# Optimization experiments

Hardware: AMD Instinct MI355X
Metric: run time of the kernel (lower is better)

The kernel has to match this reference:

```python
import jax, jax.numpy as jnp
import numpy as np

NEG = -1e9  # masked-out (non-edge) additive bias


def _attn_head(seq, bias_mat, W1, a1, b1, a2, b2, W2, bW):
    # seq: [B,N,F]; W1: [F,H]; a1,a2: [H]; W2: [H,K]
    fts = jnp.einsum('bnf,fh->bnh', seq, W1)            # Conv1D(out_sz,1,no bias)
    f1 = jnp.einsum('bnh,h->bn', fts, a1) + b1          # Conv1D(1,1)
    f2 = jnp.einsum('bnh,h->bn', fts, a2) + b2          # Conv1D(1,1)
    logits = f1[:, :, None] + f2[:, None, :]            # [B,N,N] additive attention
    coefs = jax.nn.softmax(jax.nn.leaky_relu(logits, 0.2) + bias_mat, axis=-1)
    vals = jnp.einsum('bnm,bmh->bnh', coefs, fts)       # weighted aggregation
    return jnp.einsum('bnh,hk->bnk', vals, W2) + bW     # bias_add_layer1 (Dense)


def setup_inputs() -> dict:
    B, N, F, H, NH, C = 1, 4096, 512, 64, 8, 40
    key = jax.random.key(0)
    ks = jax.random.split(key, 12)
    seq = jax.random.normal(ks[0], (B, N, F), dtype=jnp.float32)
    adj = jax.random.bernoulli(ks[1], 0.01, (B, N, N)) | jnp.eye(N, dtype=bool)[None]
    bias_mat = jnp.where(adj, 0.0, NEG).astype(jnp.float32)
    s = 0.05
    # 8 stacked first-layer heads (out_sz=H)
    W1 = jax.random.normal(ks[2], (NH, F, H), dtype=jnp.float32) * s
    a1 = jax.random.normal(ks[3], (NH, H), dtype=jnp.float32) * s
    b1 = jnp.zeros((NH,), jnp.float32)
    a2 = jax.random.normal(ks[4], (NH, H), dtype=jnp.float32) * s
    b2 = jnp.zeros((NH,), jnp.float32)
    W2 = jax.random.normal(ks[5], (NH, H, H), dtype=jnp.float32) * s
    bW = jnp.zeros((NH, H), jnp.float32)
    # single output head (out_sz=nb_classes, identity activation)
    Wo1 = jax.random.normal(ks[6], (NH * H, C), dtype=jnp.float32) * s
    ao1 = jax.random.normal(ks[7], (C,), dtype=jnp.float32) * s
    bo1 = jnp.zeros((), jnp.float32)
    ao2 = jax.random.normal(ks[8], (C,), dtype=jnp.float32) * s
    bo2 = jnp.zeros((), jnp.float32)
    Wo2 = jax.random.normal(ks[9], (C, C), dtype=jnp.float32) * s
    bo = jnp.zeros((C,), jnp.float32)
    return dict(seq=seq, bias_mat=bias_mat, W1=W1, a1=a1, b1=b1, a2=a2, b2=b2,
                W2=W2, bW=bW, Wo1=Wo1, ao1=ao1, bo1=bo1, ao2=ao2, bo2=bo2,
                Wo2=Wo2, bo=bo)


def reference(seq, bias_mat, W1, a1, b1, a2, b2, W2, bW,
              Wo1, ao1, bo1, ao2, bo2, Wo2, bo):
    # first layer: 8 heads with elu activation, vmapped over head params
    heads = jax.vmap(
        lambda w1, v1, c1, v2, c2, w2, bw: jax.nn.elu(
            _attn_head(seq, bias_mat, w1, v1, c1, v2, c2, w2, bw))
    )(W1, a1, b1, a2, b2, W2, bW)                        # [NH,B,N,H]
    NH, B, N, H = heads.shape
    h1 = jnp.moveaxis(heads, 0, 2).reshape(B, N, NH * H)  # concat along features
    # output layer: 1 head, identity activation, averaged over n_heads[-1]=1
    out = _attn_head(h1, bias_mat, Wo1, ao1, bo1, ao2, bo2, Wo2, bo)
    return out / 1.0
```

## Files before the change

kernel.cpp:

```cpp
#include <hip/hip_runtime.h>
#include <cstdint>
#include <cstddef>

#define NN 4096
#define FDIM 512
#define HDIM 64
#define NHEAD 8
#define CDIM 40
#define MAXD 256

typedef __attribute__((ext_vector_type(8))) short bf16x8;
typedef __attribute__((ext_vector_type(16))) float f32x16;

__device__ __forceinline__ float wave_max64(float v) {
  for (int o = 32; o; o >>= 1) v = fmaxf(v, __shfl_xor(v, o));
  return v;
}
__device__ __forceinline__ float wave_sum64(float v) {
  for (int o = 32; o; o >>= 1) v += __shfl_xor(v, o);
  return v;
}
__device__ __forceinline__ float readlane_f(float v, int sl) {
  return __uint_as_float((unsigned)__builtin_amdgcn_readlane((int)__float_as_uint(v), sl));
}
__device__ __forceinline__ int readlane_i(int v, int sl) {
  return __builtin_amdgcn_readlane(v, sl);
}
__device__ __forceinline__ unsigned short f2bf(float x) {
  unsigned u = __float_as_uint(x);
  return (unsigned short)((u + 0x7fffu + ((u >> 16) & 1u)) >> 16);
}
__device__ __forceinline__ float bf2f(unsigned short b) {
  return __uint_as_float(((unsigned)b) << 16);
}

__global__ __launch_bounds__(256) void k_prep(
    const float* __restrict__ bias, int* __restrict__ nbr, int* __restrict__ cnt,
    const float* __restrict__ seq, short* __restrict__ Ahi, short* __restrict__ Alo,
    const float* __restrict__ W1, short* __restrict__ Bhi, short* __restrict__ Blo,
    const float* __restrict__ W2, short* __restrict__ W2thi, short* __restrict__ W2tlo,
    const float* __restrict__ Wo1, short* __restrict__ Wo1thi, short* __restrict__ Wo1tlo) {
  __shared__ int wtot[4];
  __shared__ float T[64][65];
  int bx = blockIdx.x, tid = threadIdx.x;
  if (bx < NN) {
    int row = bx;
    int lane = tid & 63, wv = tid >> 6;
    const float4* r = (const float4*)(bias + (size_t)row * NN);
    unsigned mask = 0;
#pragma unroll
    for (int i = 0; i < 4; ++i) {
      float4 v = r[tid * 4 + i];
      mask |= (unsigned)((v.x == 0.f ? 1 : 0) | (v.y == 0.f ? 2 : 0) |
                         (v.z == 0.f ? 4 : 0) | (v.w == 0.f ? 8 : 0)) << (i * 4);
    }
    int c = __popc(mask);
    int pre = c;
#pragma unroll
    for (int o = 1; o < 64; o <<= 1) {
      int u = __shfl_up(pre, o);
      if (lane >= o) pre += u;
    }
    if (lane == 63) wtot[wv] = pre;
    __syncthreads();
    int woff = 0;
#pragma unroll
    for (int w = 0; w < 4; ++w)
      if (w < wv) woff += wtot[w];
    int excl = woff + pre - c;
    int* out = nbr + (size_t)row * MAXD;
    int col0 = tid * 16, k = 0;
#pragma unroll
    for (int i = 0; i < 16; ++i) {
      if ((mask >> i) & 1) {
        int p = excl + k;
        if (p < MAXD) out[p] = col0 + i;
        ++k;
      }
    }
    if (tid == 0) {
      int total = wtot[0] + wtot[1] + wtot[2] + wtot[3];
      cnt[row] = total < MAXD ? total : MAXD;
    }
    return;
  }
  bx -= NN;
  if (bx < 1024) {
    size_t off = (size_t)bx * 2048 + (size_t)tid * 8;
    float4 v0 = *(const float4*)(seq + off);
    float4 v1 = *(const float4*)(seq + off + 4);
    unsigned short h0 = f2bf(v0.x), h1 = f2bf(v0.y), h2 = f2bf(v0.z), h3 = f2bf(v0.w);
    unsigned short h4 = f2bf(v1.x), h5 = f2bf(v1.y), h6 = f2bf(v1.z), h7 = f2bf(v1.w);
    *(uint4*)(Ahi + off) = make_uint4(
        (unsigned)h0 | ((unsigned)h1 << 16), (unsigned)h2 | ((unsigned)h3 << 16),
        (unsigned)h4 | ((unsigned)h5 << 16), (unsigned)h6 | ((unsigned)h7 << 16));
    unsigned short l0 = f2bf(v0.x - bf2f(h0)), l1 = f2bf(v0.y - bf2f(h1));
    unsigned short l2 = f2bf(v0.z - bf2f(h2)), l3 = f2bf(v0.w - bf2f(h3));
    unsigned short l4 = f2bf(v1.x - bf2f(h4)), l5 = f2bf(v1.y - bf2f(h5));
    unsigned short l6 = f2bf(v1.z - bf2f(h6)), l7 = f2bf(v1.w - bf2f(h7));
    *(uint4*)(Alo + off) = make_uint4(
        (unsigned)l0 | ((unsigned)l1 << 16), (unsigned)l2 | ((unsigned)l3 << 16),
        (unsigned)l4 | ((unsigned)l5 << 16), (unsigned)l6 | ((unsigned)l7 << 16));
    return;
  }
  bx -= 1024;
  if (bx < 64) {
    int h = bx >> 3, kb = bx & 7;
    const float* src = W1 + ((size_t)h * FDIM + kb * 64) * HDIM;
#pragma unroll
    for (int q = 0; q < 4; ++q) {
      int fi = q * 256 + tid, kk = fi >> 4, n4 = fi & 15;
      float4 v = *(const float4*)(src + (size_t)kk * HDIM + n4 * 4);
      T[n4 * 4 + 0][kk] = v.x; T[n4 * 4 + 1][kk] = v.y;
      T[n4 * 4 + 2][kk] = v.z; T[n4 * 4 + 3][kk] = v.w;
    }
    __syncthreads();
#pragma unroll
    for (int q = 0; q < 4; ++q) {
      int fi = q * 256 + tid, n = fi >> 4, k4 = fi & 15;
      float a = T[n][k4 * 4], b = T[n][k4 * 4 + 1];
      float c = T[n][k4 * 4 + 2], d = T[n][k4 * 4 + 3];
      size_t o = ((size_t)h * 64 + n) * FDIM + kb * 64 + k4 * 4;
      unsigned short ha = f2bf(a), hb = f2bf(b), hc = f2bf(c), hd = f2bf(d);
      *(short4*)(Bhi + o) = make_short4((short)ha, (short)hb, (short)hc, (short)hd);
      *(short4*)(Blo + o) = make_short4((short)f2bf(a - bf2f(ha)), (short)f2bf(b - bf2f(hb)),
                                        (short)f2bf(c - bf2f(hc)), (short)f2bf(d - bf2f(hd)));
    }
    return;
  }
  bx -= 64;
  if (bx < 8) {
    int h = bx;
    const float* src = W2 + (size_t)h * HDIM * HDIM;
#pragma unroll
    for (int q = 0; q < 4; ++q) {
      int fi = q * 256 + tid, kk = fi >> 4, n4 = fi & 15;
      float4 v = *(const float4*)(src + (size_t)kk * HDIM + n4 * 4);
      T[n4 * 4 + 0][kk] = v.x; T[n4 * 4 + 1][kk] = v.y;
      T[n4 * 4 + 2][kk] = v.z; T[n4 * 4 + 3][kk] = v.w;
    }
    __syncthreads();
#pragma unroll
    for (int q = 0; q < 4; ++q) {
      int fi = q * 256 + tid, n = fi >> 4, k4 = fi & 15;
      float a = T[n][k4 * 4], b = T[n][k4 * 4 + 1];
      float c = T[n][k4 * 4 + 2], d = T[n][k4 * 4 + 3];
      size_t o = (size_t)h * 4096 + (size_t)n * 64 + k4 * 4;
      unsigned short ha = f2bf(a), hb = f2bf(b), hc = f2bf(c), hd = f2bf(d);
      *(short4*)(W2thi + o) = make_short4((short)ha, (short)hb, (short)hc, (short)hd);
      *(short4*)(W2tlo + o) = make_short4((short)f2bf(a - bf2f(ha)), (short)f2bf(b - bf2f(hb)),
                                          (short)f2bf(c - bf2f(hc)), (short)f2bf(d - bf2f(hd)));
    }
    return;
  }
  bx -= 8;
  {
#pragma unroll
    for (int q = 0; q < 16; ++q) {
      int idx = q * 256 + tid;
      int n = bx * 8 + (idx >> 9), k = idx & 511;
      float v = (n < CDIM) ? Wo1[(size_t)k * CDIM + n] : 0.f;
      unsigned short hv = f2bf(v);
      Wo1thi[(size_t)n * FDIM + k] = (short)hv;
      Wo1tlo[(size_t)n * FDIM + k] = (short)f2bf(v - bf2f(hv));
    }
  }
}

__global__ __launch_bounds__(256) void k_gemm(
    const short* __restrict__ Ahi, const short* __restrict__ Alo,
    const short* __restrict__ Bhi, const short* __restrict__ Blo,
    const float* __restrict__ a1, const float* __restrict__ b1,
    const float* __restrict__ a2, const float* __restrict__ b2,
    float* __restrict__ FTS, float* __restrict__ F1t, float* __restrict__ F2t) {
  __shared__ short AH[4][64][16], AL[4][64][16];
  __shared__ short BH[4][128][16], BL[4][128][16];
  const int mtile = blockIdx.x, npair = blockIdx.y;
  const int tid = threadIdx.x, lane = tid & 63, w = tid >> 6;
  const int wm = w >> 1, wn = w & 1;
  const int ml = lane & 31, g = lane >> 5, g8 = g * 8;

  f32x16 acc0, acc1;
#pragma unroll
  for (int r = 0; r < 16; ++r) { acc0[r] = 0.f; acc1[r] = 0.f; }

  const short* Abh = Ahi + (((size_t)mtile * 64) << 9);
  const short* Abl = Alo + (((size_t)mtile * 64) << 9);
  const short* Bbh = Bhi + (((size_t)npair * 128) << 9);
  const short* Bbl = Blo + (((size_t)npair * 128) << 9);

  const int tn = tid >> 3, k8 = tid & 7;
  const int ks = k8 >> 1, ko = (k8 & 1) * 8;
  const size_t so = ((size_t)tn << 9) + (size_t)k8 * 8;

  int4 rah0, rah1, ral0, ral1, rbh0, rbh1, rbh2, rbh3, rbl0, rbl1, rbl2, rbl3;
  {
    rah0 = *(const int4*)(Abh + so);              ral0 = *(const int4*)(Abl + so);
    rah1 = *(const int4*)(Abh + so + (32 << 9));  ral1 = *(const int4*)(Abl + so + (32 << 9));
    rbh0 = *(const int4*)(Bbh + so);              rbl0 = *(const int4*)(Bbl + so);
    rbh1 = *(const int4*)(Bbh + so + (32 << 9));  rbl1 = *(const int4*)(Bbl + so + (32 << 9));
    rbh2 = *(const int4*)(Bbh + so + (64 << 9));  rbl2 = *(const int4*)(Bbl + so + (64 << 9));
    rbh3 = *(const int4*)(Bbh + so + (96 << 9));  rbl3 = *(const int4*)(Bbl + so + (96 << 9));
  }

  const int NCH = FDIM / 64;
  for (int c = 0; c < NCH; ++c) {
    *(int4*)&AH[ks][tn][ko] = rah0;       *(int4*)&AL[ks][tn][ko] = ral0;
    *(int4*)&AH[ks][32 + tn][ko] = rah1;  *(int4*)&AL[ks][32 + tn][ko] = ral1;
    *(int4*)&BH[ks][tn][ko] = rbh0;       *(int4*)&BL[ks][tn][ko] = rbl0;
    *(int4*)&BH[ks][32 + tn][ko] = rbh1;  *(int4*)&BL[ks][32 + tn][ko] = rbl1;
    *(int4*)&BH[ks][64 + tn][ko] = rbh2;  *(int4*)&BL[ks][64 + tn][ko] = rbl2;
    *(int4*)&BH[ks][96 + tn][ko] = rbh3;  *(int4*)&BL[ks][96 + tn][ko] = rbl3;
    __syncthreads();
    if (c + 1 < NCH) {
      size_t o = so + (size_t)(c + 1) * 64;
      rah0 = *(const int4*)(Abh + o);              ral0 = *(const int4*)(Abl + o);
      rah1 = *(const int4*)(Abh + o + (32 << 9));  ral1 = *(const int4*)(Abl + o + (32 << 9));
      rbh0 = *(const int4*)(Bbh + o);              rbl0 = *(const int4*)(Bbl + o);
      rbh1 = *(const int4*)(Bbh + o + (32 << 9));  rbl1 = *(const int4*)(Bbl + o + (32 << 9));
      rbh2 = *(const int4*)(Bbh + o + (64 << 9));  rbl2 = *(const int4*)(Bbl + o + (64 << 9));
      rbh3 = *(const int4*)(Bbh + o + (96 << 9));  rbl3 = *(const int4*)(Bbl + o + (96 << 9));
    }
#pragma unroll
    for (int t = 0; t < 4; ++t) {
      bf16x8 ah = *(const bf16x8*)&AH[t][wm * 32 + ml][g8];
      bf16x8 al = *(const bf16x8*)&AL[t][wm * 32 + ml][g8];
      bf16x8 bh0 = *(const bf16x8*)&BH[t][wn * 64 + ml][g8];
      bf16x8 bl0 = *(const bf16x8*)&BL[t][wn * 64 + ml][g8];
      acc0 = __builtin_amdgcn_mfma_f32_32x32x16_bf16(ah, bh0, acc0, 0, 0, 0);
      acc0 = __builtin_amdgcn_mfma_f32_32x32x16_bf16(al, bh0, acc0, 0, 0, 0);
      acc0 = __builtin_amdgcn_mfma_f32_32x32x16_bf16(ah, bl0, acc0, 0, 0, 0);
      bf16x8 bh1 = *(const bf16x8*)&BH[t][wn * 64 + 32 + ml][g8];
      bf16x8 bl1 = *(const bf16x8*)&BL[t][wn * 64 + 32 + ml][g8];
      acc1 = __builtin_amdgcn_mfma_f32_32x32x16_bf16(ah, bh1, acc1, 0, 0, 0);
      acc1 = __builtin_amdgcn_mfma_f32_32x32x16_bf16(al, bh1, acc1, 0, 0, 0);
      acc1 = __builtin_amdgcn_mfma_f32_32x32x16_bf16(ah, bl1, acc1, 0, 0, 0);
    }
    __syncthreads();
  }

  const int h = npair * 2 + wn;
  const float a1lo = a1[h * 64 + ml], a1hi = a1[h * 64 + 32 + ml];
  const float a2lo = a2[h * 64 + ml], a2hi = a2[h * 64 + 32 + ml];
  const float b1h = b1[h], b2h = b2[h];
  const int row0 = mtile * 64 + wm * 32 + 4 * g;
  const int col0 = npair * 128 + wn * 64 + ml;
#pragma unroll
  for (int r = 0; r < 16; ++r) {
    int row = row0 + (r & 3) + 8 * (r >> 2);
    FTS[(size_t)row * FDIM + col0] = acc0[r];
    FTS[(size_t)row * FDIM + col0 + 32] = acc1[r];
    float p1 = acc0[r] * a1lo + acc1[r] * a1hi;
    float p2 = acc0[r] * a2lo + acc1[r] * a2hi;
#pragma unroll
    for (int o = 1; o < 32; o <<= 1) {
      p1 += __shfl_xor(p1, o);
      p2 += __shfl_xor(p2, o);
    }
    if (ml == 0) {
      F1t[(size_t)row * 8 + h] = p1 + b1h;
      F2t[(size_t)row * 8 + h] = p2 + b2h;
    }
  }
}

__global__ __launch_bounds__(256) void k_agg1(
    const float* __restrict__ FTS, const float* __restrict__ F1t,
    const float* __restrict__ F2t, const int* __restrict__ nbr,
    const int* __restrict__ cnt, short* __restrict__ VALShi,
    short* __restrict__ VALSlo) {
  int wv = threadIdx.x >> 6, lane = threadIdx.x & 63;
  int gw = blockIdx.x * 4 + wv;
  int i = gw >> 1, hg = gw & 1;
  int deg = cnt[i];
  const int* nb = nbr + (size_t)i * MAXD;
  float4 f1v = *(const float4*)(F1t + (size_t)i * 8 + hg * 4);

  float4 p4[4];
  int jreg[4];
  float mx = -1e30f, my = -1e30f, mz = -1e30f, mw = -1e30f;
#pragma unroll
  for (int r = 0; r < 4; ++r) {
    int t = r * 64 + lane;
    jreg[r] = 0;
    p4[r] = make_float4(-1e30f, -1e30f, -1e30f, -1e30f);
    if (t < deg) {
      int j = nb[t];
      jreg[r] = j;
      float4 f2v = *(const float4*)(F2t + (size_t)j * 8 + hg * 4);
      float4 x;
      x.x = f1v.x + f2v.x; x.x = x.x >= 0.f ? x.x : 0.2f * x.x;
      x.y = f1v.y + f2v.y; x.y = x.y >= 0.f ? x.y : 0.2f * x.y;
      x.z = f1v.z + f2v.z; x.z = x.z >= 0.f ? x.z : 0.2f * x.z;
      x.w = f1v.w + f2v.w; x.w = x.w >= 0.f ? x.w : 0.2f * x.w;
      p4[r] = x;
      mx = fmaxf(mx, x.x); my = fmaxf(my, x.y);
      mz = fmaxf(mz, x.z); mw = fmaxf(mw, x.w);
    }
  }
  mx = wave_max64(mx); my = wave_max64(my);
  mz = wave_max64(mz); mw = wave_max64(mw);
  float sx = 0.f, sy = 0.f, sz = 0.f, sw = 0.f;
#pragma unroll
  for (int r = 0; r < 4; ++r) {
    int t = r * 64 + lane;
    float4 e = make_float4(0.f, 0.f, 0.f, 0.f);
    if (t < deg) {
      e.x = __expf(p4[r].x - mx); e.y = __expf(p4[r].y - my);
      e.z = __expf(p4[r].z - mz); e.w = __expf(p4[r].w - mw);
    }
    p4[r] = e;
    sx += e.x; sy += e.y; sz += e.z; sw += e.w;
  }
  sx = wave_sum64(sx); sy = wave_sum64(sy);
  sz = wave_sum64(sz); sw = wave_sum64(sw);

  int q = lane >> 4;
  float invh = (q < 2) ? (q == 0 ? 1.f / sx : 1.f / sy)
                       : (q == 2 ? 1.f / sz : 1.f / sw);

  float4 accA = make_float4(0.f, 0.f, 0.f, 0.f);
  float4 accB = make_float4(0.f, 0.f, 0.f, 0.f);
  const float* Fb = FTS + hg * 256;
#pragma unroll
  for (int r = 0; r < 4; ++r) {
    int base = r * 64;
    if (base >= deg) break;
    int lim = deg - base;
    lim = lim < 64 ? lim : 64;
    int sl = 0;
    for (; sl + 2 <= lim; sl += 2) {
      int j0 = readlane_i(jreg[r], sl);
      int j1 = readlane_i(jreg[r], sl + 1);
      float w00 = readlane_f(p4[r].x, sl),     w01 = readlane_f(p4[r].y, sl);
      float w02 = readlane_f(p4[r].z, sl),     w03 = readlane_f(p4[r].w, sl);
      float w10 = readlane_f(p4[r].x, sl + 1), w11 = readlane_f(p4[r].y, sl + 1);
      float w12 = readlane_f(p4[r].z, sl + 1), w13 = readlane_f(p4[r].w, sl + 1);
      float wA = (q < 2) ? (q == 0 ? w00 : w01) : (q == 2 ? w02 : w03);
      float wB = (q < 2) ? (q == 0 ? w10 : w11) : (q == 2 ? w12 : w13);
      float4 f0 = *(const float4*)(Fb + (size_t)j0 * FDIM + lane * 4);
      float4 f1 = *(const float4*)(Fb + (size_t)j1 * FDIM + lane * 4);
      accA.x += wA * f0.x; accA.y += wA * f0.y; accA.z += wA * f0.z; accA.w += wA * f0.w;
      accB.x += wB * f1.x; accB.y += wB * f1.y; accB.z += wB * f1.z; accB.w += wB * f1.w;
    }
    if (sl < lim) {
      int j0 = readlane_i(jreg[r], sl);
      float w00 = readlane_f(p4[r].x, sl), w01 = readlane_f(p4[r].y, sl);
      float w02 = readlane_f(p4[r].z, sl), w03 = readlane_f(p4[r].w, sl);
      float wA = (q < 2) ? (q == 0 ? w00 : w01) : (q == 2 ? w02 : w03);
      float4 f0 = *(const float4*)(Fb + (size_t)j0 * FDIM + lane * 4);
      accA.x += wA * f0.x; accA.y += wA * f0.y; accA.z += wA * f0.z; accA.w += wA * f0.w;
    }
  }
  float vx = (accA.x + accB.x) * invh, vy = (accA.y + accB.y) * invh;
  float vz = (accA.z + accB.z) * invh, vw = (accA.w + accB.w) * invh;
  unsigned short hx = f2bf(vx), hy = f2bf(vy), hz = f2bf(vz), hw = f2bf(vw);
  size_t o = (size_t)i * FDIM + hg * 256 + lane * 4;
  *(short4*)(VALShi + o) = make_short4((short)hx, (short)hy, (short)hz, (short)hw);
  *(short4*)(VALSlo + o) = make_short4(
      (short)f2bf(vx - bf2f(hx)), (short)f2bf(vy - bf2f(hy)),
      (short)f2bf(vz - bf2f(hz)), (short)f2bf(vw - bf2f(hw)));
}

__global__ __launch_bounds__(256) void k_w2(
    const short* __restrict__ VALShi, const short* __restrict__ VALSlo,
    const short* __restrict__ W2thi, const short* __restrict__ W2tlo,
    const float* __restrict__ bW, short* __restrict__ H1hi, short* __restrict__ H1lo) {
  __shared__ short AH[4][64][16], AL[4][64][16];
  __shared__ short BH[4][64][16], BL[4][64][16];
  const int rb = blockIdx.x, h = blockIdx.y;
  const int tid = threadIdx.x, lane = tid & 63, w = tid >> 6;
  const int wm = w >> 1, wn = w & 1;
  const int ml = lane & 31, g = lane >> 5, g8 = g * 8;
  const int tn = tid >> 2, k8 = tid & 3;
  {
    const short* pa = VALShi + ((size_t)(rb * 64 + tn) << 9) + h * 64 + k8 * 16;
    const short* pl = VALSlo + ((size_t)(rb * 64 + tn) << 9) + h * 64 + k8 * 16;
    *(int4*)&AH[k8][tn][0] = *(const int4*)pa;
    *(int4*)&AH[k8][tn][8] = *(const int4*)(pa + 8);
    *(int4*)&AL[k8][tn][0] = *(const int4*)pl;
    *(int4*)&AL[k8][tn][8] = *(const int4*)(pl + 8);
    const short* pb = W2thi + (size_t)h * 4096 + tn * 64 + k8 * 16;
    const short* pbl = W2tlo + (size_t)h * 4096 + tn * 64 + k8 * 16;
    *(int4*)&BH[k8][tn][0] = *(const int4*)pb;
    *(int4*)&BH[k8][tn][8] = *(const int4*)(pb + 8);
    *(int4*)&BL[k8][tn][0] = *(const int4*)pbl;
    *(int4*)&BL[k8][tn][8] = *(const int4*)(pbl + 8);
  }
  __syncthreads();
  f32x16 acc;
#pragma unroll
  for (int r = 0; r < 16; ++r) acc[r] = 0.f;
#pragma unroll
  for (int t = 0; t < 4; ++t) {
    bf16x8 ah = *(const bf16x8*)&AH[t][wm * 32 + ml][g8];
    bf16x8 al = *(const bf16x8*)&AL[t][wm * 32 + ml][g8];
    bf16x8 bh = *(const bf16x8*)&BH[t][wn * 32 + ml][g8];
    bf16x8 bl = *(const bf16x8*)&BL[t][wn * 32 + ml][g8];
    acc = __builtin_amdgcn_mfma_f32_32x32x16_bf16(ah, bh, acc, 0, 0, 0);
    acc = __builtin_amdgcn_mfma_f32_32x32x16_bf16(al, bh, acc, 0, 0, 0);
    acc = __builtin_amdgcn_mfma_f32_32x32x16_bf16(ah, bl, acc, 0, 0, 0);
  }
  const int col = wn * 32 + ml;
  const float bwv = bW[h * 64 + col];
  const int row0 = rb * 64 + wm * 32 + 4 * g;
#pragma unroll
  for (int r = 0; r < 16; ++r) {
    int row = row0 + (r & 3) + 8 * (r >> 2);
    float v = acc[r] + bwv;
    v = v > 0.f ? v : __expf(v) - 1.f;
    unsigned short hv = f2bf(v);
    size_t o = ((size_t)row << 9) + h * 64 + col;
    H1hi[o] = (short)hv;
    H1lo[o] = (short)f2bf(v - bf2f(hv));
  }
}

__global__ __launch_bounds__(256) void k_fts2(
    const short* __restrict__ H1hi, const short* __restrict__ H1lo,
    const short* __restrict__ Wo1thi, const short* __restrict__ Wo1tlo,
    const float* __restrict__ ao1, const float* __restrict__ bo1s,
    const float* __restrict__ ao2, const float* __restrict__ bo2s,
    float* __restrict__ FTS2, float* __restrict__ F1O, float* __restrict__ F2O) {
  __shared__ short AH[4][64][16], AL[4][64][16];
  __shared__ short BH[4][64][16], BL[4][64][16];
  __shared__ float p1buf[2][64], p2buf[2][64];
  const int i0 = blockIdx.x * 64;
  const int tid = threadIdx.x, lane = tid & 63, w = tid >> 6;
  const int wm = w >> 1, wn = w & 1;
  const int ml = lane & 31, g = lane >> 5, g8 = g * 8;
  const int tn = tid >> 2, k8 = tid & 3;

  f32x16 acc;
#pragma unroll
  for (int r = 0; r < 16; ++r) acc[r] = 0.f;

  for (int c = 0; c < 8; ++c) {
    const size_t ka = ((size_t)(i0 + tn) << 9) + c * 64 + k8 * 16;
    *(int4*)&AH[k8][tn][0] = *(const int4*)(H1hi + ka);
    *(int4*)&AH[k8][tn][8] = *(const int4*)(H1hi + ka + 8);
    *(int4*)&AL[k8][tn][0] = *(const int4*)(H1lo + ka);
    *(int4*)&AL[k8][tn][8] = *(const int4*)(H1lo + ka + 8);
    const size_t kb = ((size_t)tn << 9) + c * 64 + k8 * 16;
    *(int4*)&BH[k8][tn][0] = *(const int4*)(Wo1thi + kb);
    *(int4*)&BH[k8][tn][8] = *(const int4*)(Wo1thi + kb + 8);
    *(int4*)&BL[k8][tn][0] = *(const int4*)(Wo1tlo + kb);
    *(int4*)&BL[k8][tn][8] = *(const int4*)(Wo1tlo + kb + 8);
    __syncthreads();
#pragma unroll
    for (int t = 0; t < 4; ++t) {
      bf16x8 ah = *(const bf16x8*)&AH[t][wm * 32 + ml][g8];
      bf16x8 al = *(const bf16x8*)&AL[t][wm * 32 + ml][g8];
      bf16x8 bh = *(const bf16x8*)&BH[t][wn * 32 + ml][g8];
      bf16x8 bl = *(const bf16x8*)&BL[t][wn * 32 + ml][g8];
      acc = __builtin_amdgcn_mfma_f32_32x32x16_bf16(ah, bh, acc, 0, 0, 0);
      acc = __builtin_amdgcn_mfma_f32_32x32x16_bf16(al, bh, acc, 0, 0, 0);
      acc = __builtin_amdgcn_mfma_f32_32x32x16_bf16(ah, bl, acc, 0, 0, 0);
    }
    __syncthreads();
  }

  const int col = wn * 32 + ml;
  const bool act = col < CDIM;
  const float aov1 = act ? ao1[col] : 0.f;
  const float aov2 = act ? ao2[col] : 0.f;
  const int lrow0 = wm * 32 + 4 * g;
#pragma unroll
  for (int r = 0; r < 16; ++r) {
    int lrow = lrow0 + (r & 3) + 8 * (r >> 2);
    float v = acc[r];
    if (act) FTS2[(size_t)(i0 + lrow) * CDIM + col] = v;
    float p1 = v * aov1, p2 = v * aov2;
#pragma unroll
    for (int o = 1; o < 32; o <<= 1) {
      p1 += __shfl_xor(p1, o);
      p2 += __shfl_xor(p2, o);
    }
    if (ml == 0) {
      p1buf[wn][lrow] = p1;
      p2buf[wn][lrow] = p2;
    }
  }
  __syncthreads();
  if (tid < 64) {
    F1O[i0 + tid] = p1buf[0][tid] + p1buf[1][tid] + bo1s[0];
    F2O[i0 + tid] = p2buf[0][tid] + p2buf[1][tid] + bo2s[0];
  }
}

__global__ __launch_bounds__(256) void k_agg2(
    const float* __restrict__ FTS2, const float* __restrict__ F1O,
    const float* __restrict__ F2O, const int* __restrict__ nbr,
    const int* __restrict__ cnt, const float* __restrict__ Wo2,
    const float* __restrict__ bo, float* __restrict__ out) {
  int i = blockIdx.x * 4 + (threadIdx.x >> 6);
  int lane = threadIdx.x & 63;
  int deg = cnt[i];
  const int* nb = nbr + (size_t)i * MAXD;
  float f1i = F1O[i];

  int jreg[4];
  float p[4];
  float m = -1e30f;
#pragma unroll
  for (int r = 0; r < 4; ++r) { jreg[r] = 0; p[r] = -1e30f; }
#pragma unroll
  for (int r = 0; r < 4; ++r) {
    int t = r * 64 + lane;
    if (t < deg) {
      int j = nb[t];
      jreg[r] = j;
      float x = f1i + F2O[j];
      x = x >= 0.f ? x : 0.2f * x;
      p[r] = x;
      m = fmaxf(m, x);
    }
  }
  m = wave_max64(m);
  float s = 0.f;
#pragma unroll
  for (int r = 0; r < 4; ++r) {
    int t = r * 64 + lane;
    float e = (t < deg) ? __expf(p[r] - m) : 0.f;
    p[r] = e;
    s += e;
  }
  s = wave_sum64(s);

  const bool act = lane < CDIM;
  float acc = 0.f;
#pragma unroll
  for (int r = 0; r < 4; ++r) {
    int base = r * 64;
    if (base >= deg) break;
    int lim = deg - base;
    lim = lim < 64 ? lim : 64;
    for (int sl = 0; sl < lim; ++sl) {
      float w = readlane_f(p[r], sl);
      int j   = readlane_i(jreg[r], sl);
      float fv = act ? FTS2[(size_t)j * CDIM + lane] : 0.f;
      acc += w * fv;
    }
  }
  float v = acc / s;

  float o = act ? bo[lane] : 0.f;
  for (int kk = 0; kk < CDIM; ++kk) {
    float w = readlane_f(v, kk);
    float b = act ? Wo2[kk * CDIM + lane] : 0.f;
    o += w * b;
  }
  if (act) out[(size_t)i * CDIM + lane] = o;
}

extern "C" void kernel_launch(void* const* d_in, const int* in_sizes, int n_in,
                              void* d_out, int out_size, void* d_ws, size_t ws_size,
                              hipStream_t stream) {
  const float* seq  = (const float*)d_in[0];
  const float* bias = (const float*)d_in[1];
  const float* W1   = (const float*)d_in[2];
  const float* a1   = (const float*)d_in[3];
  const float* b1   = (const float*)d_in[4];
  const float* a2   = (const float*)d_in[5];
  const float* b2   = (const float*)d_in[6];
  const float* W2   = (const float*)d_in[7];
  const float* bW   = (const float*)d_in[8];
  const float* Wo1  = (const float*)d_in[9];
  const float* ao1  = (const float*)d_in[10];
  const float* bo1  = (const float*)d_in[11];
  const float* ao2  = (const float*)d_in[12];
  const float* bo2  = (const float*)d_in[13];
  const float* Wo2  = (const float*)d_in[14];
  const float* bo   = (const float*)d_in[15];
  float* out = (float*)d_out;

  float* ws    = (float*)d_ws;
  float* FTS   = ws;
  float* F1t   = FTS  + (size_t)NN * FDIM;
  float* F2t   = F1t  + (size_t)NN * NHEAD;
  float* FTS2  = F2t  + (size_t)NN * NHEAD;
  float* F1O   = FTS2 + (size_t)NN * CDIM;
  float* F2O   = F1O  + NN;
  short* Ahi   = (short*)(F2O + NN);
  short* Alo   = Ahi + (size_t)NN * FDIM;
  short* Bhi   = Alo + (size_t)NN * FDIM;
  short* Blo   = Bhi + (size_t)NHEAD * HDIM * FDIM;
  short* VALShi= Blo + (size_t)NHEAD * HDIM * FDIM;
  short* VALSlo= VALShi + (size_t)NN * FDIM;
  short* H1hi  = VALSlo + (size_t)NN * FDIM;
  short* H1lo  = H1hi + (size_t)NN * FDIM;
  short* W2thi = H1lo + (size_t)NN * FDIM;
  short* W2tlo = W2thi + (size_t)NHEAD * HDIM * HDIM;
  short* Wo1thi= W2tlo + (size_t)NHEAD * HDIM * HDIM;
  short* Wo1tlo= Wo1thi + (size_t)64 * FDIM;
  int*   nbr   = (int*)(Wo1tlo + (size_t)64 * FDIM);
  int*   cnt   = nbr + (size_t)NN * MAXD;

  k_prep<<<NN + 1024 + 64 + 8 + 8, 256, 0, stream>>>(
      bias, nbr, cnt, seq, Ahi, Alo, W1, Bhi, Blo, W2, W2thi, W2tlo,
      Wo1, Wo1thi, Wo1tlo);
  k_gemm<<<dim3(NN / 64, NHEAD / 2), 256, 0, stream>>>(
      Ahi, Alo, Bhi, Blo, a1, b1, a2, b2, FTS, F1t, F2t);
  k_agg1<<<NN * 2 / 4, 256, 0, stream>>>(FTS, F1t, F2t, nbr, cnt, VALShi, VALSlo);
  k_w2<<<dim3(NN / 64, NHEAD), 256, 0, stream>>>(VALShi, VALSlo, W2thi, W2tlo,
                                                 bW, H1hi, H1lo);
  k_fts2<<<NN / 64, 256, 0, stream>>>(H1hi, H1lo, Wo1thi, Wo1tlo,
                                      ao1, bo1, ao2, bo2, FTS2, F1O, F2O);
  k_agg2<<<NN / 4, 256, 0, stream>>>(FTS2, F1O, F2O, nbr, cnt, Wo2, bo, out);
}
```

Before: 101.9 us.

## Fuse W2 projection and output-layer GEMM into one tail kernel; LDS softmax weights

Merges the per-head W2 dense layer (with ELU) and the output-layer Wo1 GEMM into a single kernel. Each head's H1 tile stays in shared memory as hi/lo bf16 and is consumed immediately, which removes the H1 hi/lo round trip through global memory and one launch. It also stores softmax weights in LDS in agg1 instead of using per-edge readlanes with selects, and splits agg2's gather into two accumulators to get more loads in flight. The trade is fewer blocks in the fused kernel (64 instead of 512 for the W2 step) and extra shared memory and barriers.

```diff
diff --git a/kernel.cpp b/kernel.cpp
--- a/kernel.cpp
+++ b/kernel.cpp
@@ -269,6 +269,7 @@
     const float* __restrict__ F2t, const int* __restrict__ nbr,
     const int* __restrict__ cnt, short* __restrict__ VALShi,
     short* __restrict__ VALSlo) {
+  __shared__ float plds[4][MAXD][4];
   int wv = threadIdx.x >> 6, lane = threadIdx.x & 63;
   int gw = blockIdx.x * 4 + wv;
   int i = gw >> 1, hg = gw & 1;
@@ -311,6 +312,7 @@
     }
     p4[r] = e;
     sx += e.x; sy += e.y; sz += e.z; sw += e.w;
+    *(float4*)&plds[wv][r * 64 + lane][0] = e;
   }
   sx = wave_sum64(sx); sy = wave_sum64(sy);
   sz = wave_sum64(sz); sw = wave_sum64(sw);
@@ -332,12 +334,8 @@
     for (; sl + 2 <= lim; sl += 2) {
       int j0 = readlane_i(jreg[r], sl);
       int j1 = readlane_i(jreg[r], sl + 1);
-      float w00 = readlane_f(p4[r].x, sl),     w01 = readlane_f(p4[r].y, sl);
-      float w02 = readlane_f(p4[r].z, sl),     w03 = readlane_f(p4[r].w, sl);
-      float w10 = readlane_f(p4[r].x, sl + 1), w11 = readlane_f(p4[r].y, sl + 1);
-      float w12 = readlane_f(p4[r].z, sl + 1), w13 = readlane_f(p4[r].w, sl + 1);
-      float wA = (q < 2) ? (q == 0 ? w00 : w01) : (q == 2 ? w02 : w03);
-      float wB = (q < 2) ? (q == 0 ? w10 : w11) : (q == 2 ? w12 : w13);
+      float wA = plds[wv][base + sl][q];
+      float wB = plds[wv][base + sl + 1][q];
       float4 f0 = *(const float4*)(Fb + (size_t)j0 * FDIM + lane * 4);
       float4 f1 = *(const float4*)(Fb + (size_t)j1 * FDIM + lane * 4);
       accA.x += wA * f0.x; accA.y += wA * f0.y; accA.z += wA * f0.z; accA.w += wA * f0.w;
@@ -345,9 +343,7 @@
     }
     if (sl < lim) {
       int j0 = readlane_i(jreg[r], sl);
-      float w00 = readlane_f(p4[r].x, sl), w01 = readlane_f(p4[r].y, sl);
-      float w02 = readlane_f(p4[r].z, sl), w03 = readlane_f(p4[r].w, sl);
-      float wA = (q < 2) ? (q == 0 ? w00 : w01) : (q == 2 ? w02 : w03);
+      float wA = plds[wv][base + sl][q];
       float4 f0 = *(const float4*)(Fb + (size_t)j0 * FDIM + lane * 4);
       accA.x += wA * f0.x; accA.y += wA * f0.y; accA.z += wA * f0.z; accA.w += wA * f0.w;
     }
@@ -362,114 +358,99 @@
       (short)f2bf(vz - bf2f(hz)), (short)f2bf(vw - bf2f(hw)));
 }
 
-__global__ __launch_bounds__(256) void k_w2(
+__global__ __launch_bounds__(256) void k_tail(
     const short* __restrict__ VALShi, const short* __restrict__ VALSlo,
     const short* __restrict__ W2thi, const short* __restrict__ W2tlo,
-    const float* __restrict__ bW, short* __restrict__ H1hi, short* __restrict__ H1lo) {
-  __shared__ short AH[4][64][16], AL[4][64][16];
-  __shared__ short BH[4][64][16], BL[4][64][16];
-  const int rb = blockIdx.x, h = blockIdx.y;
-  const int tid = threadIdx.x, lane = tid & 63, w = tid >> 6;
-  const int wm = w >> 1, wn = w & 1;
-  const int ml = lane & 31, g = lane >> 5, g8 = g * 8;
-  const int tn = tid >> 2, k8 = tid & 3;
-  {
-    const short* pa = VALShi + ((size_t)(rb * 64 + tn) << 9) + h * 64 + k8 * 16;
-    const short* pl = VALSlo + ((size_t)(rb * 64 + tn) << 9) + h * 64 + k8 * 16;
-    *(int4*)&AH[k8][tn][0] = *(const int4*)pa;
-    *(int4*)&AH[k8][tn][8] = *(const int4*)(pa + 8);
-    *(int4*)&AL[k8][tn][0] = *(const int4*)pl;
-    *(int4*)&AL[k8][tn][8] = *(const int4*)(pl + 8);
-    const short* pb = W2thi + (size_t)h * 4096 + tn * 64 + k8 * 16;
-    const short* pbl = W2tlo + (size_t)h * 4096 + tn * 64 + k8 * 16;
-    *(int4*)&BH[k8][tn][0] = *(const int4*)pb;
-    *(int4*)&BH[k8][tn][8] = *(const int4*)(pb + 8);
-    *(int4*)&BL[k8][tn][0] = *(const int4*)pbl;
-    *(int4*)&BL[k8][tn][8] = *(const int4*)(pbl + 8);
-  }
-  __syncthreads();
-  f32x16 acc;
-#pragma unroll
-  for (int r = 0; r < 16; ++r) acc[r] = 0.f;
-#pragma unroll
-  for (int t = 0; t < 4; ++t) {
-    bf16x8 ah = *(const bf16x8*)&AH[t][wm * 32 + ml][g8];
-    bf16x8 al = *(const bf16x8*)&AL[t][wm * 32 + ml][g8];
-    bf16x8 bh = *(const bf16x8*)&BH[t][wn * 32 + ml][g8];
-    bf16x8 bl = *(const bf16x8*)&BL[t][wn * 32 + ml][g8];
-    acc = __builtin_amdgcn_mfma_f32_32x32x16_bf16(ah, bh, acc, 0, 0, 0);
-    acc = __builtin_amdgcn_mfma_f32_32x32x16_bf16(al, bh, acc, 0, 0, 0);
-    acc = __builtin_amdgcn_mfma_f32_32x32x16_bf16(ah, bl, acc, 0, 0, 0);
-  }
-  const int col = wn * 32 + ml;
-  const float bwv = bW[h * 64 + col];
-  const int row0 = rb * 64 + wm * 32 + 4 * g;
-#pragma unroll
-  for (int r = 0; r < 16; ++r) {
-    int row = row0 + (r & 3) + 8 * (r >> 2);
-    float v = acc[r] + bwv;
-    v = v > 0.f ? v : __expf(v) - 1.f;
-    unsigned short hv = f2bf(v);
-    size_t o = ((size_t)row << 9) + h * 64 + col;
-    H1hi[o] = (short)hv;
-    H1lo[o] = (short)f2bf(v - bf2f(hv));
-  }
-}
-
-__global__ __launch_bounds__(256) void k_fts2(
-    const short* __restrict__ H1hi, const short* __restrict__ H1lo,
+    const float* __restrict__ bW,
     const short* __restrict__ Wo1thi, const short* __restrict__ Wo1tlo,
     const float* __restrict__ ao1, const float* __restrict__ bo1s,
     const float* __restrict__ ao2, const float* __restrict__ bo2s,
     float* __restrict__ FTS2, float* __restrict__ F1O, float* __restrict__ F2O) {
   __shared__ short AH[4][64][16], AL[4][64][16];
   __shared__ short BH[4][64][16], BL[4][64][16];
+  __shared__ short CH[4][64][16], CL[4][64][16];
+  __shared__ short DH[4][64][16], DL[4][64][16];
   __shared__ float p1buf[2][64], p2buf[2][64];
   const int i0 = blockIdx.x * 64;
   const int tid = threadIdx.x, lane = tid & 63, w = tid >> 6;
   const int wm = w >> 1, wn = w & 1;
   const int ml = lane & 31, g = lane >> 5, g8 = g * 8;
   const int tn = tid >> 2, k8 = tid & 3;
-
-  f32x16 acc;
-#pragma unroll
-  for (int r = 0; r < 16; ++r) acc[r] = 0.f;
-
-  for (int c = 0; c < 8; ++c) {
-    const size_t ka = ((size_t)(i0 + tn) << 9) + c * 64 + k8 * 16;
-    *(int4*)&AH[k8][tn][0] = *(const int4*)(H1hi + ka);
-    *(int4*)&AH[k8][tn][8] = *(const int4*)(H1hi + ka + 8);
-    *(int4*)&AL[k8][tn][0] = *(const int4*)(H1lo + ka);
-    *(int4*)&AL[k8][tn][8] = *(const int4*)(H1lo + ka + 8);
-    const size_t kb = ((size_t)tn << 9) + c * 64 + k8 * 16;
-    *(int4*)&BH[k8][tn][0] = *(const int4*)(Wo1thi + kb);
-    *(int4*)&BH[k8][tn][8] = *(const int4*)(Wo1thi + kb + 8);
-    *(int4*)&BL[k8][tn][0] = *(const int4*)(Wo1tlo + kb);
-    *(int4*)&BL[k8][tn][8] = *(const int4*)(Wo1tlo + kb + 8);
-    __syncthreads();
+  const int colw = wn * 32 + ml;
+  const int rowl0 = wm * 32 + 4 * g;
+
+  f32x16 acc2;
+#pragma unroll
+  for (int r = 0; r < 16; ++r) acc2[r] = 0.f;
+
+  for (int h = 0; h < NHEAD; ++h) {
+    {
+      const short* pa = VALShi + ((size_t)(i0 + tn) << 9) + h * 64 + k8 * 16;
+      const short* pl = VALSlo + ((size_t)(i0 + tn) << 9) + h * 64 + k8 * 16;
+      *(int4*)&AH[k8][tn][0] = *(const int4*)pa;
+      *(int4*)&AH[k8][tn][8] = *(const int4*)(pa + 8);
+      *(int4*)&AL[k8][tn][0] = *(const int4*)pl;
+      *(int4*)&AL[k8][tn][8] = *(const int4*)(pl + 8);
+      const short* pb  = W2thi + (size_t)h * 4096 + tn * 64 + k8 * 16;
+      const short* pbl = W2tlo + (size_t)h * 4096 + tn * 64 + k8 * 16;
+      *(int4*)&BH[k8][tn][0] = *(const int4*)pb;
+      *(int4*)&BH[k8][tn][8] = *(const int4*)(pb + 8);
+      *(int4*)&BL[k8][tn][0] = *(const int4*)pbl;
+      *(int4*)&BL[k8][tn][8] = *(const int4*)(pbl + 8);
+      const short* pd  = Wo1thi + (size_t)tn * FDIM + h * 64 + k8 * 16;
+      const short* pdl = Wo1tlo + (size_t)tn * FDIM + h * 64 + k8 * 16;
+      *(int4*)&DH[k8][tn][0] = *(const int4*)pd;
+      *(int4*)&DH[k8][tn][8] = *(const int4*)(pd + 8);
+      *(int4*)&DL[k8][tn][0] = *(const int4*)pdl;
+      *(int4*)&DL[k8][tn][8] = *(const int4*)(pdl + 8);
+    }
+    __syncthreads();
+    f32x16 accw;
+#pragma unroll
+    for (int r = 0; r < 16; ++r) accw[r] = 0.f;
 #pragma unroll
     for (int t = 0; t < 4; ++t) {
       bf16x8 ah = *(const bf16x8*)&AH[t][wm * 32 + ml][g8];
       bf16x8 al = *(const bf16x8*)&AL[t][wm * 32 + ml][g8];
       bf16x8 bh = *(const bf16x8*)&BH[t][wn * 32 + ml][g8];
       bf16x8 bl = *(const bf16x8*)&BL[t][wn * 32 + ml][g8];
-      acc = __builtin_amdgcn_mfma_f32_32x32x16_bf16(ah, bh, acc, 0, 0, 0);
-      acc = __builtin_amdgcn_mfma_f32_32x32x16_bf16(al, bh, acc, 0, 0, 0);
-      acc = __builtin_amdgcn_mfma_f32_32x32x16_bf16(ah, bl, acc, 0, 0, 0);
-    }
-    __syncthreads();
-  }
-
-  const int col = wn * 32 + ml;
-  const bool act = col < CDIM;
-  const float aov1 = act ? ao1[col] : 0.f;
-  const float aov2 = act ? ao2[col] : 0.f;
-  const int lrow0 = wm * 32 + 4 * g;
+      accw = __builtin_amdgcn_mfma_f32_32x32x16_bf16(ah, bh, accw, 0, 0, 0);
+      accw = __builtin_amdgcn_mfma_f32_32x32x16_bf16(al, bh, accw, 0, 0, 0);
+      accw = __builtin_amdgcn_mfma_f32_32x32x16_bf16(ah, bl, accw, 0, 0, 0);
+    }
+    const float bwv = bW[h * 64 + colw];
+    const int ts = colw >> 4, ss = colw & 15;
+#pragma unroll
+    for (int r = 0; r < 16; ++r) {
+      int rl = rowl0 + (r & 3) + 8 * (r >> 2);
+      float v = accw[r] + bwv;
+      v = v > 0.f ? v : __expf(v) - 1.f;
+      unsigned short hv = f2bf(v);
+      CH[ts][rl][ss] = (short)hv;
+      CL[ts][rl][ss] = (short)f2bf(v - bf2f(hv));
+    }
+    __syncthreads();
+#pragma unroll
+    for (int t = 0; t < 4; ++t) {
+      bf16x8 ah = *(const bf16x8*)&CH[t][wm * 32 + ml][g8];
+      bf16x8 al = *(const bf16x8*)&CL[t][wm * 32 + ml][g8];
+      bf16x8 bh = *(const bf16x8*)&DH[t][wn * 32 + ml][g8];
+      bf16x8 bl = *(const bf16x8*)&DL[t][wn * 32 + ml][g8];
+      acc2 = __builtin_amdgcn_mfma_f32_32x32x16_bf16(ah, bh, acc2, 0, 0, 0);
+      acc2 = __builtin_amdgcn_mfma_f32_32x32x16_bf16(al, bh, acc2, 0, 0, 0);
+      acc2 = __builtin_amdgcn_mfma_f32_32x32x16_bf16(ah, bl, acc2, 0, 0, 0);
+    }
+    __syncthreads();
+  }
+
+  const bool act = colw < CDIM;
+  const float aov1 = act ? ao1[colw] : 0.f;
+  const float aov2 = act ? ao2[colw] : 0.f;
 #pragma unroll
   for (int r = 0; r < 16; ++r) {
-    int lrow = lrow0 + (r & 3) + 8 * (r >> 2);
-    float v = acc[r];
-    if (act) FTS2[(size_t)(i0 + lrow) * CDIM + col] = v;
+    int rl = rowl0 + (r & 3) + 8 * (r >> 2);
+    float v = acc2[r];
+    if (act) FTS2[(size_t)(i0 + rl) * CDIM + colw] = v;
     float p1 = v * aov1, p2 = v * aov2;
 #pragma unroll
     for (int o = 1; o < 32; o <<= 1) {
@@ -477,8 +458,8 @@
       p2 += __shfl_xor(p2, o);
     }
     if (ml == 0) {
-      p1buf[wn][lrow] = p1;
-      p2buf[wn][lrow] = p2;
+      p1buf[wn][rl] = p1;
+      p2buf[wn][rl] = p2;
     }
   }
   __syncthreads();
@@ -528,21 +509,32 @@
   s = wave_sum64(s);
 
   const bool act = lane < CDIM;
-  float acc = 0.f;
+  float accA = 0.f, accB = 0.f;
 #pragma unroll
   for (int r = 0; r < 4; ++r) {
     int base = r * 64;
     if (base >= deg) break;
     int lim = deg - base;
     lim = lim < 64 ? lim : 64;
-    for (int sl = 0; sl < lim; ++sl) {
-      float w = readlane_f(p[r], sl);
-      int j   = readlane_i(jreg[r], sl);
-      float fv = act ? FTS2[(size_t)j * CDIM + lane] : 0.f;
-      acc += w * fv;
-    }
-  }
-  float v = acc / s;
+    int sl = 0;
+    for (; sl + 2 <= lim; sl += 2) {
+      float w0 = readlane_f(p[r], sl);
+      float w1 = readlane_f(p[r], sl + 1);
+      int j0 = readlane_i(jreg[r], sl);
+      int j1 = readlane_i(jreg[r], sl + 1);
+      float f0 = act ? FTS2[(size_t)j0 * CDIM + lane] : 0.f;
+      float f1 = act ? FTS2[(size_t)j1 * CDIM + lane] : 0.f;
+      accA += w0 * f0;
+      accB += w1 * f1;
+    }
+    if (sl < lim) {
+      float w0 = readlane_f(p[r], sl);
+      int j0 = readlane_i(jreg[r], sl);
+      float f0 = act ? FTS2[(size_t)j0 * CDIM + lane] : 0.f;
+      accA += w0 * f0;
+    }
+  }
+  float v = (accA + accB) / s;
 
   float o = act ? bo[lane] : 0.f;
   for (int kk = 0; kk < CDIM; ++kk) {
@@ -587,9 +579,7 @@
   short* Blo   = Bhi + (size_t)NHEAD * HDIM * FDIM;
   short* VALShi= Blo + (size_t)NHEAD * HDIM * FDIM;
   short* VALSlo= VALShi + (size_t)NN * FDIM;
-  short* H1hi  = VALSlo + (size_t)NN * FDIM;
-  short* H1lo  = H1hi + (size_t)NN * FDIM;
-  short* W2thi = H1lo + (size_t)NN * FDIM;
+  short* W2thi = VALSlo + (size_t)NN * FDIM;
   short* W2tlo = W2thi + (size_t)NHEAD * HDIM * HDIM;
   short* Wo1thi= W2tlo + (size_t)NHEAD * HDIM * HDIM;
   short* Wo1tlo= Wo1thi + (size_t)64 * FDIM;
@@ -602,9 +592,8 @@
   k_gemm<<<dim3(NN / 64, NHEAD / 2), 256, 0, stream>>>(
       Ahi, Alo, Bhi, Blo, a1, b1, a2, b2, FTS, F1t, F2t);
   k_agg1<<<NN * 2 / 4, 256, 0, stream>>>(FTS, F1t, F2t, nbr, cnt, VALShi, VALSlo);
-  k_w2<<<dim3(NN / 64, NHEAD), 256, 0, stream>>>(VALShi, VALSlo, W2thi, W2tlo,
-                                                 bW, H1hi, H1lo);
-  k_fts2<<<NN / 64, 256, 0, stream>>>(H1hi, H1lo, Wo1thi, Wo1tlo,
-                                      ao1, bo1, ao2, bo2, FTS2, F1O, F2O);
+  k_tail<<<NN / 64, 256, 0, stream>>>(VALShi, VALSlo, W2thi, W2tlo, bW,
+                                      Wo1thi, Wo1tlo, ao1, bo1, ao2, bo2,
+                                      FTS2, F1O, F2O);
   k_agg2<<<NN / 4, 256, 0, stream>>>(FTS2, F1O, F2O, nbr, cnt, Wo2, bo, out);
 }
```

Measured after the change: 101.8 us. About the same (-0.1%).
